# Optimization experiments

Hardware: AMD Instinct MI355X
Metric: run time of the kernel (lower is better)

The kernel has to match this reference:

```python
import jax, jax.numpy as jnp
import numpy as np

B, N, D = 32, 2048, 512

def setup_inputs() -> dict:
    key = jax.random.key(0)
    k1, k2, k3, k4 = jax.random.split(key, 4)
    return {
        "src": jax.random.normal(k1, (B, N, 3), dtype=jnp.float32),
        "tgt": jax.random.normal(k2, (B, N, 3), dtype=jnp.float32),
        "src_embed": jax.random.normal(k3, (B, N, D), dtype=jnp.float32),
        "tgt_embed": jax.random.normal(k4, (B, N, D), dtype=jnp.float32),
    }

def reference(src, tgt, src_embed, tgt_embed):
    # src, tgt: (B, N, 3); src_embed, tgt_embed: (B, N, D)
    d_k = jnp.asarray(src_embed.shape[-1], dtype=src_embed.dtype)
    # attention scores (B, N_src, N_tgt), softmax over tgt points
    scores = jnp.einsum('bnd,bmd->bnm', src_embed, tgt_embed) / jnp.sqrt(d_k)
    pointer = jax.nn.softmax(scores, axis=2)
    # matched = tgt^T @ pointer^T -> (B, 3, N_src)
    matched = jnp.einsum('bmc,bnm->bcn', tgt, pointer)
    src_t = jnp.transpose(src, (0, 2, 1))  # (B, 3, N)
    src_cent = jnp.mean(src_t, axis=2, keepdims=True)        # (B, 3, 1)
    matched_cent = jnp.mean(matched, axis=2, keepdims=True)  # (B, 3, 1)
    src_demean = src_t - src_cent
    matched_demean = matched - matched_cent
    # cross-covariance H: (B, 3, 3)
    H = jnp.einsum('bcn,bdn->bcd', src_demean, matched_demean)
    U, _, Vh = jnp.linalg.svd(H, full_matrices=False)  # square 3x3: reduced == full
    V = jnp.transpose(Vh, (0, 2, 1))
    R = jnp.matmul(V, jnp.transpose(U, (0, 2, 1)))
    det = jnp.linalg.det(R)
    identity = jnp.eye(3, dtype=R.dtype)
    reflect = jnp.diag(jnp.array([1.0, 1.0, -1.0], dtype=R.dtype))
    refl = jnp.where((det >= 0)[:, None, None], identity, reflect)
    R = jnp.matmul(refl, R)
    t = jnp.matmul(-R, src_cent) + matched_cent  # (B, 3, 1)
    t = jnp.transpose(t, (0, 2, 1))              # (B, 1, 3)
    return (R, t)
```

## Files before the change

kernel.cpp:

```cpp
#include <hip/hip_runtime.h>
#include <hip/hip_fp16.h>
#include <math.h>

#define B_ 32
#define N_ 2048
#define D_ 512
#define NT 256

typedef __attribute__((ext_vector_type(8))) _Float16 f16x8;
typedef __attribute__((ext_vector_type(8))) short s16x8;
typedef __attribute__((ext_vector_type(4))) float f32x4;
typedef __attribute__((ext_vector_type(4))) unsigned int u32x4;

__device__ inline unsigned packh2(float lo, float hi) {
    __half l = __float2half_rn(lo), h = __float2half_rn(hi);
    return (unsigned)__half_as_ushort(l) | ((unsigned)__half_as_ushort(h) << 16);
}
__device__ inline unsigned f2bf(float x) {
    unsigned u = __float_as_uint(x);
    return (u + 0x7FFFu + ((u >> 16) & 1u)) >> 16;
}
__device__ inline float bf2f(unsigned h) { return __uint_as_float(h << 16); }

__global__ __launch_bounds__(256) void prepass_kernel(
    const float* __restrict__ te, u32x4* __restrict__ kp)
{
    const int idx = blockIdx.x * 256 + threadIdx.x;
    const int b   = idx >> 17;
    const int r17 = idx & 131071;
    const int mt  = r17 >> 13;
    const int kt  = (r17 >> 9) & 15;
    const int o16 = r17 & 511;
    const int r   = o16 >> 2;
    const int s   = o16 & 3;
    const int lg  = s ^ ((r >> 1) & 3);
    const float* src = te + (((size_t)b * N_ + mt * 128 + r) * D_ + kt * 32 + lg * 8);
    const float4 f0 = *(const float4*)src;
    const float4 f1 = *(const float4*)(src + 4);
    u32x4 u;
    u[0] = packh2(f0.x, f0.y);
    u[1] = packh2(f0.z, f0.w);
    u[2] = packh2(f1.x, f1.y);
    u[3] = packh2(f1.z, f1.w);
    kp[idx] = u;
}

__global__ __launch_bounds__(NT, 2) void attn_db_kernel(
    const float* __restrict__ src, const float* __restrict__ tgt,
    const float* __restrict__ src_embed, const u32x4* __restrict__ kp,
    float* __restrict__ partials)
{
    __shared__ f16x8 Kbuf[2][4][512];
    __shared__ float4 TsB[2][128];
    __shared__ double red[4][15];

    const int tid  = threadIdx.x;
    const int wv   = tid >> 6;
    const int lane = tid & 63;
    const int lr   = lane & 15;
    const int lg   = lane >> 4;
    const int sxb  = (lg ^ ((lr >> 1) & 3)) << 4;
    char* KbufB = (char*)&Kbuf[0][0][0];

    const int xcd  = blockIdx.x & 7;
    const int idx  = blockIdx.x >> 3;
    const int b    = xcd * 4 + (idx >> 4);
    const int msl  = idx & 15;
    const int n0   = msl * 128;
    const int pblk = b * 16 + msl;

    const float QSC = 0.044194173824159216f * 1.4426950408889634f;
    f16x8 Qr[2][16];
#pragma unroll
    for (int qf = 0; qf < 2; ++qf) {
        const int qrow = n0 + wv * 32 + qf * 16 + lr;
        const float* qp = src_embed + ((size_t)b * N_ + qrow) * D_ + lg * 8;
#pragma unroll
        for (int s = 0; s < 16; ++s) {
            const float4 f0 = *(const float4*)(qp + s * 32);
            const float4 f1 = *(const float4*)(qp + s * 32 + 4);
            u32x4 u;
            u[0] = packh2(f0.x * QSC, f0.y * QSC);
            u[1] = packh2(f0.z * QSC, f0.w * QSC);
            u[2] = packh2(f1.x * QSC, f1.y * QSC);
            u[3] = packh2(f1.z * QSC, f1.w * QSC);
            Qr[qf][s] = __builtin_bit_cast(f16x8, u);
        }
    }
    if (tid < 128) {
        const float* tp = tgt + ((size_t)b * N_ + tid) * 3;
        TsB[0][tid] = make_float4(tp[0], tp[1], tp[2], 0.f);
    }

#define STAGE_TILE(t_, half_, ti_) do {                                        \
    const u32x4* _g = kp +                                                     \
        ((((size_t)b * 16 + ((t_) >> 4)) * 16 + ((t_) & 15)) << 9);            \
    __builtin_amdgcn_global_load_lds(                                          \
        (const __attribute__((address_space(1))) void*)(_g + tid),             \
        (__attribute__((address_space(3))) void*)(&Kbuf[half_][ti_][wv * 64]), \
        16, 0, 0);                                                             \
    __builtin_amdgcn_global_load_lds(                                          \
        (const __attribute__((address_space(1))) void*)(_g + 256 + tid),       \
        (__attribute__((address_space(3))) void*)(&Kbuf[half_][ti_][256 + wv * 64]),\
        16, 0, 0);                                                             \
} while (0)

#define STAGE_GROUP(gi_, half_) do {                                           \
    STAGE_TILE(4 * (gi_) + 0, half_, 0);                                       \
    STAGE_TILE(4 * (gi_) + 1, half_, 1);                                       \
    STAGE_TILE(4 * (gi_) + 2, half_, 2);                                       \
    STAGE_TILE(4 * (gi_) + 3, half_, 3);                                       \
} while (0)

    STAGE_GROUP(0, 0);

    float m_s[2] = {-1e30f, -1e30f}, l_s[2] = {0.f, 0.f};
    float axs[2] = {0.f, 0.f}, ays[2] = {0.f, 0.f}, azs[2] = {0.f, 0.f};

    f32x4 acc0[8], acc1[8];

    for (int g4 = 0; g4 < 16; ++g4) {
#pragma unroll
        for (int gm = 0; gm < 4; ++gm) {
            const int g = (g4 << 2) | gm;
            __syncthreads();
            if (g < 63) {
                const int gn = g + 1;
                STAGE_GROUP(gn, gn & 1);
            }
            float tv0 = 0.f, tv1 = 0.f, tv2 = 0.f;
            const bool pf = (gm == 3) && (g4 < 15) && (tid < 128);
            if (pf) {
                const float* tp = tgt + ((size_t)b * N_ + (g4 + 1) * 128 + tid) * 3;
                tv0 = tp[0]; tv1 = tp[1]; tv2 = tp[2];
            }
            if (gm == 0) {
#pragma unroll
                for (int nf = 0; nf < 8; ++nf) {
                    acc0[nf] = (f32x4){0.f, 0.f, 0.f, 0.f};
                    acc1[nf] = (f32x4){0.f, 0.f, 0.f, 0.f};
                }
            }
            __builtin_amdgcn_s_setprio(1);
#pragma unroll
            for (int ti = 0; ti < 4; ++ti) {
                const int kt = (gm << 2) | ti;
                const char* abase = KbufB + ((g & 1) << 15) + (ti << 13)
                                  + lr * 64 + sxb;
#pragma unroll
                for (int nf = 0; nf < 8; ++nf) {
                    const f16x8 a = *(const f16x8*)(abase + nf * 1024);
                    acc0[nf] = __builtin_amdgcn_mfma_f32_16x16x32_f16(a, Qr[0][kt], acc0[nf], 0, 0, 0);
                    acc1[nf] = __builtin_amdgcn_mfma_f32_16x16x32_f16(a, Qr[1][kt], acc1[nf], 0, 0, 0);
                }
            }
            __builtin_amdgcn_s_setprio(0);
            if (pf)
                TsB[(g4 + 1) & 1][tid] = make_float4(tv0, tv1, tv2, 0.f);

            if (gm == 3) {
                const float4* Ts = &TsB[g4 & 1][0];
                float mx0 = -1e30f, mx1 = -1e30f;
#pragma unroll
                for (int nf = 0; nf < 8; ++nf)
#pragma unroll
                    for (int r4 = 0; r4 < 4; ++r4) {
                        mx0 = fmaxf(mx0, acc0[nf][r4]);
                        mx1 = fmaxf(mx1, acc1[nf][r4]);
                    }
                mx0 = fmaxf(mx0, __shfl_xor(mx0, 16)); mx0 = fmaxf(mx0, __shfl_xor(mx0, 32));
                mx1 = fmaxf(mx1, __shfl_xor(mx1, 16)); mx1 = fmaxf(mx1, __shfl_xor(mx1, 32));
                const float mn0 = fmaxf(m_s[0], mx0), mn1 = fmaxf(m_s[1], mx1);
                const float c0 = exp2f(m_s[0] - mn0), c1 = exp2f(m_s[1] - mn1);
                l_s[0] *= c0; axs[0] *= c0; ays[0] *= c0; azs[0] *= c0; m_s[0] = mn0;
                l_s[1] *= c1; axs[1] *= c1; ays[1] *= c1; azs[1] *= c1; m_s[1] = mn1;
                float l0 = 0.f, x0 = 0.f, y0 = 0.f, z0 = 0.f;
                float l1 = 0.f, x1 = 0.f, y1 = 0.f, z1 = 0.f;
#pragma unroll
                for (int nf = 0; nf < 8; ++nf)
#pragma unroll
                    for (int r4 = 0; r4 < 4; ++r4) {
                        const float4 tv = Ts[nf * 16 + lg * 4 + r4];
                        const float p0 = exp2f(acc0[nf][r4] - mn0);
                        const float p1 = exp2f(acc1[nf][r4] - mn1);
                        l0 += p0; x0 = fmaf(p0, tv.x, x0); y0 = fmaf(p0, tv.y, y0); z0 = fmaf(p0, tv.z, z0);
                        l1 += p1; x1 = fmaf(p1, tv.x, x1); y1 = fmaf(p1, tv.y, y1); z1 = fmaf(p1, tv.z, z1);
                    }
                l_s[0] += l0; axs[0] += x0; ays[0] += y0; azs[0] += z0;
                l_s[1] += l1; axs[1] += x1; ays[1] += y1; azs[1] += z1;
            }
        }
    }
#undef STAGE_GROUP
#undef STAGE_TILE

    double dl[15];
#pragma unroll
    for (int i = 0; i < 15; ++i) dl[i] = 0.0;
#pragma unroll
    for (int qf = 0; qf < 2; ++qf) {
        float lt = l_s[qf], x = axs[qf], y = ays[qf], z = azs[qf];
        lt += __shfl_xor(lt, 16); lt += __shfl_xor(lt, 32);
        x  += __shfl_xor(x, 16);  x  += __shfl_xor(x, 32);
        y  += __shfl_xor(y, 16);  y  += __shfl_xor(y, 32);
        z  += __shfl_xor(z, 16);  z  += __shfl_xor(z, 32);
        if (lg == 0) {
            const int qrow = n0 + wv * 32 + qf * 16 + lr;
            const float* sp = src + ((size_t)b * N_ + qrow) * 3;
            const double inv = 1.0 / (double)lt;
            const double m0d = (double)x * inv, m1d = (double)y * inv, m2d = (double)z * inv;
            const double s0 = sp[0], s1 = sp[1], s2 = sp[2];
            dl[0] += s0;  dl[1] += s1;  dl[2] += s2;
            dl[3] += m0d; dl[4] += m1d; dl[5] += m2d;
            dl[6]  += s0 * m0d; dl[7]  += s0 * m1d; dl[8]  += s0 * m2d;
            dl[9]  += s1 * m0d; dl[10] += s1 * m1d; dl[11] += s1 * m2d;
            dl[12] += s2 * m0d; dl[13] += s2 * m1d; dl[14] += s2 * m2d;
        }
    }
#pragma unroll
    for (int i = 0; i < 15; ++i) {
        double v = dl[i];
        for (int off = 1; off < 64; off <<= 1) v += __shfl_xor(v, off);
        dl[i] = v;
    }
    if (lane == 0) {
#pragma unroll
        for (int i = 0; i < 15; ++i) red[wv][i] = dl[i];
    }
    __syncthreads();
    if (tid < 15) {
        double sum = 0.0;
        for (int w = 0; w < 4; ++w) sum += red[w][tid];
        partials[(size_t)pblk * 15 + tid] = (float)sum;
    }
}

__global__ __launch_bounds__(256, 2) void attn_v2_kernel(
    const float* __restrict__ src, const float* __restrict__ tgt,
    const float* __restrict__ src_embed, const float* __restrict__ tgt_embed,
    float* __restrict__ partials)
{
    __shared__ short Khi_s[128 * 64];
    __shared__ short Klo_s[128 * 64];
    __shared__ float4 Ts4[128];
    __shared__ double red[64][15];

    char* KhiB = (char*)Khi_s;
    char* KloB = (char*)Klo_s;

    const int w    = blockIdx.x;
    const int xcd  = w & 7;
    const int idx  = w >> 3;
    const int b    = xcd * 4 + (idx >> 5);
    const int n0   = (idx & 31) * 64;
    const int blk  = b * 32 + (idx & 31);

    const int tid  = threadIdx.x;
    const int wv   = tid >> 6;
    const int lane = tid & 63;
    const int lr   = lane & 15;
    const int lg   = lane >> 4;
    const unsigned swl = (unsigned)((lr & 7) << 4);

    const float scale = 0.044194173824159216f;
    const float* kbase = tgt_embed + (size_t)b * N_ * D_;

    const int qrow = n0 + wv * 16 + lr;
    const float* qp = src_embed + ((size_t)b * N_ + qrow) * D_ + lg * 8;
    s16x8 qhi[16], qlo[16];
#pragma unroll
    for (int s = 0; s < 16; ++s) {
        const float4 f0 = *reinterpret_cast<const float4*>(qp + s * 32);
        const float4 f1 = *reinterpret_cast<const float4*>(qp + s * 32 + 4);
        const float x[8] = {f0.x, f0.y, f0.z, f0.w, f1.x, f1.y, f1.z, f1.w};
#pragma unroll
        for (int i = 0; i < 8; ++i) {
            const float v = x[i] * scale;
            const unsigned h = f2bf(v);
            qhi[s][i] = (short)h;
            qlo[s][i] = (short)f2bf(v - bf2f(h));
        }
    }

    float m_run = -1e30f, l_run = 0.f, a0 = 0.f, a1 = 0.f, a2 = 0.f;
    const int srow = tid >> 1;
    const int shalf = tid & 1;
    const unsigned swr = (unsigned)((srow & 7) << 4);

    for (int m0 = 0; m0 < N_; m0 += 128) {
        f32x4 acc[8];
#pragma unroll
        for (int nf = 0; nf < 8; ++nf) acc[nf] = (f32x4){0.f, 0.f, 0.f, 0.f};

#pragma unroll
        for (int kt = 0; kt < 8; ++kt) {
            __syncthreads();
            {
                const float* gp = kbase + (size_t)(m0 + srow) * D_ + kt * 64 + shalf * 32;
#pragma unroll
                for (int grp = 0; grp < 4; ++grp) {
                    const float4 fa = *reinterpret_cast<const float4*>(gp + grp * 8);
                    const float4 fb = *reinterpret_cast<const float4*>(gp + grp * 8 + 4);
                    const float x[8] = {fa.x, fa.y, fa.z, fa.w, fb.x, fb.y, fb.z, fb.w};
                    s16x8 hi, lo;
#pragma unroll
                    for (int i = 0; i < 8; ++i) {
                        const unsigned h = f2bf(x[i]);
                        hi[i] = (short)h;
                        lo[i] = (short)f2bf(x[i] - bf2f(h));
                    }
                    const unsigned off = (unsigned)srow * 128u +
                        (((unsigned)(shalf * 64 + grp * 16)) ^ swr);
                    *reinterpret_cast<s16x8*>(KhiB + off) = hi;
                    *reinterpret_cast<s16x8*>(KloB + off) = lo;
                }
                if (kt == 0 && tid < 128) {
                    const float* tp = tgt + ((size_t)b * N_ + m0 + tid) * 3;
                    Ts4[tid] = make_float4(tp[0], tp[1], tp[2], 0.f);
                }
            }
            __syncthreads();
#pragma unroll
            for (int ks = 0; ks < 2; ++ks) {
                const int s = kt * 2 + ks;
                const unsigned kb = ((unsigned)(lg * 16 + ks * 64)) ^ swl;
#pragma unroll
                for (int nf = 0; nf < 8; ++nf) {
                    const unsigned off = (unsigned)(nf * 16 + lr) * 128u + kb;
                    const s16x8 ah = *reinterpret_cast<const s16x8*>(KhiB + off);
                    const s16x8 al = *reinterpret_cast<const s16x8*>(KloB + off);
                    acc[nf] = __builtin_amdgcn_mfma_f32_16x16x32_bf16(ah, qhi[s], acc[nf], 0, 0, 0);
                    acc[nf] = __builtin_amdgcn_mfma_f32_16x16x32_bf16(al, qhi[s], acc[nf], 0, 0, 0);
                    acc[nf] = __builtin_amdgcn_mfma_f32_16x16x32_bf16(ah, qlo[s], acc[nf], 0, 0, 0);
                }
            }
        }

        float mx = -1e30f;
#pragma unroll
        for (int nf = 0; nf < 8; ++nf)
#pragma unroll
            for (int r = 0; r < 4; ++r) mx = fmaxf(mx, acc[nf][r]);
        mx = fmaxf(mx, __shfl_xor(mx, 16));
        mx = fmaxf(mx, __shfl_xor(mx, 32));

        const float mnew = fmaxf(m_run, mx);
        const float corr = __expf(m_run - mnew);
        l_run *= corr; a0 *= corr; a1 *= corr; a2 *= corr;

        float ps = 0.f, p0 = 0.f, p1 = 0.f, p2 = 0.f;
#pragma unroll
        for (int nf = 0; nf < 8; ++nf)
#pragma unroll
            for (int r = 0; r < 4; ++r) {
                const float p = __expf(acc[nf][r] - mnew);
                const int n = nf * 16 + lg * 4 + r;
                const float4 tv = Ts4[n];
                ps += p;
                p0 = fmaf(p, tv.x, p0);
                p1 = fmaf(p, tv.y, p1);
                p2 = fmaf(p, tv.z, p2);
            }
        l_run += ps; a0 += p0; a1 += p1; a2 += p2;
        m_run = mnew;
    }

    l_run += __shfl_xor(l_run, 16); l_run += __shfl_xor(l_run, 32);
    a0 += __shfl_xor(a0, 16); a0 += __shfl_xor(a0, 32);
    a1 += __shfl_xor(a1, 16); a1 += __shfl_xor(a1, 32);
    a2 += __shfl_xor(a2, 16); a2 += __shfl_xor(a2, 32);

    __syncthreads();
    if (lg == 0) {
        const float inv = 1.0f / l_run;
        const double mx0 = (double)(a0 * inv);
        const double mx1 = (double)(a1 * inv);
        const double mx2 = (double)(a2 * inv);
        const float* sp = src + ((size_t)b * N_ + qrow) * 3;
        const double s0 = sp[0], s1 = sp[1], s2 = sp[2];
        double* rp = red[wv * 16 + lr];
        rp[0] = s0;  rp[1] = s1;  rp[2] = s2;
        rp[3] = mx0; rp[4] = mx1; rp[5] = mx2;
        rp[6]  = s0 * mx0; rp[7]  = s0 * mx1; rp[8]  = s0 * mx2;
        rp[9]  = s1 * mx0; rp[10] = s1 * mx1; rp[11] = s1 * mx2;
        rp[12] = s2 * mx0; rp[13] = s2 * mx1; rp[14] = s2 * mx2;
    }
    __syncthreads();
    if (tid < 15) {
        double sum = 0.0;
        for (int j = 0; j < 64; ++j) sum += red[j][tid];
        partials[(size_t)blk * 15 + tid] = (float)sum;
    }
}

__global__ void kabsch_kernel(const float* __restrict__ partials,
                              float* __restrict__ out, int nbb)
{
    const int b = threadIdx.x;
    if (b >= B_) return;

    double acc[15];
#pragma unroll
    for (int i = 0; i < 15; ++i) acc[i] = 0.0;
    for (int rb = 0; rb < nbb; ++rb) {
        const float* p = partials + ((size_t)b * nbb + rb) * 15;
#pragma unroll
        for (int i = 0; i < 15; ++i) acc[i] += (double)p[i];
    }

    const double invN = 1.0 / (double)N_;
    const double S[3] = {acc[0], acc[1], acc[2]};
    const double M[3] = {acc[3], acc[4], acc[5]};
    double H[3][3];
    for (int c = 0; c < 3; ++c)
        for (int d = 0; d < 3; ++d)
            H[c][d] = acc[6 + c * 3 + d] - S[c] * M[d] * invN;

    double A[3][3];
    for (int i = 0; i < 3; ++i)
        for (int j = 0; j < 3; ++j)
            A[i][j] = H[0][i] * H[0][j] + H[1][i] * H[1][j] + H[2][i] * H[2][j];

    double V[3][3] = {{1, 0, 0}, {0, 1, 0}, {0, 0, 1}};
    const int PQ[3][2] = {{0, 1}, {0, 2}, {1, 2}};
    for (int sweep = 0; sweep < 20; ++sweep) {
        const double off = fabs(A[0][1]) + fabs(A[0][2]) + fabs(A[1][2]);
        if (off < 1e-24) break;
        for (int pi = 0; pi < 3; ++pi) {
            const int p = PQ[pi][0], q = PQ[pi][1], rr = 3 - p - q;
            const double apq = A[p][q];
            if (fabs(apq) < 1e-300) continue;
            const double theta = (A[q][q] - A[p][p]) / (2.0 * apq);
            const double tt = (theta >= 0.0 ? 1.0 : -1.0) /
                              (fabs(theta) + sqrt(1.0 + theta * theta));
            const double c = 1.0 / sqrt(1.0 + tt * tt);
            const double sn = tt * c;
            const double app = A[p][p], aqq = A[q][q];
            const double arp = A[rr][p], arq = A[rr][q];
            A[p][p] = app - tt * apq;
            A[q][q] = aqq + tt * apq;
            A[p][q] = A[q][p] = 0.0;
            A[rr][p] = A[p][rr] = c * arp - sn * arq;
            A[rr][q] = A[q][rr] = sn * arp + c * arq;
            for (int k = 0; k < 3; ++k) {
                const double vkp = V[k][p], vkq = V[k][q];
                V[k][p] = c * vkp - sn * vkq;
                V[k][q] = sn * vkp + c * vkq;
            }
        }
    }

    double R[3][3] = {{0, 0, 0}, {0, 0, 0}, {0, 0, 0}};
    for (int i = 0; i < 3; ++i) {
        const double lam = A[i][i];
        const double sig = sqrt(lam > 0.0 ? lam : 0.0);
        const double inv = 1.0 / (sig > 1e-30 ? sig : 1e-30);
        double wv[3];
        for (int c = 0; c < 3; ++c)
            wv[c] = H[c][0] * V[0][i] + H[c][1] * V[1][i] + H[c][2] * V[2][i];
        for (int r = 0; r < 3; ++r)
            for (int c = 0; c < 3; ++c)
                R[r][c] += V[r][i] * wv[c] * inv;
    }

    const double det =
        R[0][0] * (R[1][1] * R[2][2] - R[1][2] * R[2][1]) -
        R[0][1] * (R[1][0] * R[2][2] - R[1][2] * R[2][0]) +
        R[0][2] * (R[1][0] * R[2][1] - R[1][1] * R[2][0]);
    if (det < 0.0) {
        R[2][0] = -R[2][0]; R[2][1] = -R[2][1]; R[2][2] = -R[2][2];
    }

    double t[3];
    for (int c = 0; c < 3; ++c)
        t[c] = M[c] * invN -
               (R[c][0] * S[0] + R[c][1] * S[1] + R[c][2] * S[2]) * invN;

    for (int r = 0; r < 3; ++r)
        for (int c = 0; c < 3; ++c)
            out[(size_t)b * 9 + r * 3 + c] = (float)R[r][c];
    for (int c = 0; c < 3; ++c)
        out[(size_t)B_ * 9 + (size_t)b * 3 + c] = (float)t[c];
}

extern "C" void kernel_launch(void* const* d_in, const int* in_sizes, int n_in,
                              void* d_out, int out_size, void* d_ws, size_t ws_size,
                              hipStream_t stream) {
    const float* src = (const float*)d_in[0];
    const float* tgt = (const float*)d_in[1];
    const float* se  = (const float*)d_in[2];
    const float* te  = (const float*)d_in[3];
    float* out = (float*)d_out;

    const size_t KP_OFF = 32768;
    const size_t need = KP_OFF + (size_t)B_ * N_ * D_ * 2;

    if (ws_size >= need) {
        u32x4* kp = (u32x4*)((char*)d_ws + KP_OFF);
        prepass_kernel<<<dim3(16384), dim3(256), 0, stream>>>(te, kp);
        attn_db_kernel<<<dim3(512), dim3(NT), 0, stream>>>(
            src, tgt, se, kp, (float*)d_ws);
        kabsch_kernel<<<dim3(1), dim3(64), 0, stream>>>((float*)d_ws, out, 16);
    } else {
        attn_v2_kernel<<<dim3(1024), dim3(256), 0, stream>>>(
            src, tgt, se, te, (float*)d_ws);
        kabsch_kernel<<<dim3(1), dim3(64), 0, stream>>>((float*)d_ws, out, 32);
    }
}
```

Baseline: 226.5 us.

## Switch attention scores to 32x32x16 MFMA tiles per wave

Replaces the paired 16x16x32 MFMA fragments with a single 32x32x16 MFMA layout, so each wave computes a 32-query by 128-key tile with four 16-wide accumulator vectors. Q fragments, the K swizzled LDS addressing, the softmax row/column mapping and the final reductions are remapped for the new lane layout. The aim is fewer LDS reads per MFMA and fewer instructions per FLOP; in exchange it changes register pressure and the LDS access pattern.

```diff
diff --git a/kernel.cpp b/kernel.cpp
--- a/kernel.cpp
+++ b/kernel.cpp
@@ -10,6 +10,7 @@
 typedef __attribute__((ext_vector_type(8))) _Float16 f16x8;
 typedef __attribute__((ext_vector_type(8))) short s16x8;
 typedef __attribute__((ext_vector_type(4))) float f32x4;
+typedef __attribute__((ext_vector_type(16))) float f32x16;
 typedef __attribute__((ext_vector_type(4))) unsigned int u32x4;
 
 __device__ inline unsigned packh2(float lo, float hi) {
@@ -45,7 +46,7 @@
     kp[idx] = u;
 }
 
-__global__ __launch_bounds__(NT, 2) void attn_db_kernel(
+__global__ __launch_bounds__(NT, 2) void attn_db32_kernel(
     const float* __restrict__ src, const float* __restrict__ tgt,
     const float* __restrict__ src_embed, const u32x4* __restrict__ kp,
     float* __restrict__ partials)
@@ -57,10 +58,13 @@
     const int tid  = threadIdx.x;
     const int wv   = tid >> 6;
     const int lane = tid & 63;
-    const int lr   = lane & 15;
-    const int lg   = lane >> 4;
-    const int sxb  = (lg ^ ((lr >> 1) & 3)) << 4;
+    const int lr   = lane & 31;
+    const int hi   = lane >> 5;
     char* KbufB = (char*)&Kbuf[0][0][0];
+
+    const int sw   = (lr >> 1) & 3;
+    const int sxb0 = ((0 + hi) ^ sw) << 4;
+    const int sxb1 = ((2 + hi) ^ sw) << 4;
 
     const int xcd  = blockIdx.x & 7;
     const int idx  = blockIdx.x >> 3;
@@ -70,21 +74,20 @@
     const int pblk = b * 16 + msl;
 
     const float QSC = 0.044194173824159216f * 1.4426950408889634f;
-    f16x8 Qr[2][16];
-#pragma unroll
-    for (int qf = 0; qf < 2; ++qf) {
-        const int qrow = n0 + wv * 32 + qf * 16 + lr;
-        const float* qp = src_embed + ((size_t)b * N_ + qrow) * D_ + lg * 8;
-#pragma unroll
-        for (int s = 0; s < 16; ++s) {
-            const float4 f0 = *(const float4*)(qp + s * 32);
-            const float4 f1 = *(const float4*)(qp + s * 32 + 4);
+    const int qrow = n0 + wv * 32 + lr;
+    f16x8 Qr[32];
+    {
+        const float* qp = src_embed + ((size_t)b * N_ + qrow) * D_ + hi * 8;
+#pragma unroll
+        for (int s = 0; s < 32; ++s) {
+            const float4 f0 = *(const float4*)(qp + s * 16);
+            const float4 f1 = *(const float4*)(qp + s * 16 + 4);
             u32x4 u;
             u[0] = packh2(f0.x * QSC, f0.y * QSC);
             u[1] = packh2(f0.z * QSC, f0.w * QSC);
             u[2] = packh2(f1.x * QSC, f1.y * QSC);
             u[3] = packh2(f1.z * QSC, f1.w * QSC);
-            Qr[qf][s] = __builtin_bit_cast(f16x8, u);
+            Qr[s] = __builtin_bit_cast(f16x8, u);
         }
     }
     if (tid < 128) {
@@ -114,10 +117,8 @@
 
     STAGE_GROUP(0, 0);
 
-    float m_s[2] = {-1e30f, -1e30f}, l_s[2] = {0.f, 0.f};
-    float axs[2] = {0.f, 0.f}, ays[2] = {0.f, 0.f}, azs[2] = {0.f, 0.f};
-
-    f32x4 acc0[8], acc1[8];
+    float m_s = -1e30f, l_s = 0.f, axs = 0.f, ays = 0.f, azs = 0.f;
+    f32x16 acc[4];
 
     for (int g4 = 0; g4 < 16; ++g4) {
 #pragma unroll
@@ -136,22 +137,25 @@
             }
             if (gm == 0) {
 #pragma unroll
-                for (int nf = 0; nf < 8; ++nf) {
-                    acc0[nf] = (f32x4){0.f, 0.f, 0.f, 0.f};
-                    acc1[nf] = (f32x4){0.f, 0.f, 0.f, 0.f};
-                }
-            }
+                for (int rg = 0; rg < 4; ++rg)
+#pragma unroll
+                    for (int r16 = 0; r16 < 16; ++r16) acc[rg][r16] = 0.f;
+            }
+            const char* gbase = KbufB + ((g & 1) << 15) + lr * 64;
             __builtin_amdgcn_s_setprio(1);
 #pragma unroll
             for (int ti = 0; ti < 4; ++ti) {
-                const int kt = (gm << 2) | ti;
-                const char* abase = KbufB + ((g & 1) << 15) + (ti << 13)
-                                  + lr * 64 + sxb;
-#pragma unroll
-                for (int nf = 0; nf < 8; ++nf) {
-                    const f16x8 a = *(const f16x8*)(abase + nf * 1024);
-                    acc0[nf] = __builtin_amdgcn_mfma_f32_16x16x32_f16(a, Qr[0][kt], acc0[nf], 0, 0, 0);
-                    acc1[nf] = __builtin_amdgcn_mfma_f32_16x16x32_f16(a, Qr[1][kt], acc1[nf], 0, 0, 0);
+                const char* tb = gbase + (ti << 13);
+#pragma unroll
+                for (int kh = 0; kh < 2; ++kh) {
+                    const int sxb = kh ? sxb1 : sxb0;
+                    const f16x8 q = Qr[(((gm << 2) | ti) << 1) | kh];
+#pragma unroll
+                    for (int rg = 0; rg < 4; ++rg) {
+                        const f16x8 a = *(const f16x8*)(tb + rg * 2048 + sxb);
+                        acc[rg] = __builtin_amdgcn_mfma_f32_32x32x16_f16(
+                            a, q, acc[rg], 0, 0, 0);
+                    }
                 }
             }
             __builtin_amdgcn_s_setprio(0);
@@ -160,62 +164,56 @@
 
             if (gm == 3) {
                 const float4* Ts = &TsB[g4 & 1][0];
-                float mx0 = -1e30f, mx1 = -1e30f;
-#pragma unroll
-                for (int nf = 0; nf < 8; ++nf)
-#pragma unroll
-                    for (int r4 = 0; r4 < 4; ++r4) {
-                        mx0 = fmaxf(mx0, acc0[nf][r4]);
-                        mx1 = fmaxf(mx1, acc1[nf][r4]);
+                float mx = -1e30f;
+#pragma unroll
+                for (int rg = 0; rg < 4; ++rg)
+#pragma unroll
+                    for (int r16 = 0; r16 < 16; ++r16)
+                        mx = fmaxf(mx, acc[rg][r16]);
+                mx = fmaxf(mx, __shfl_xor(mx, 32));
+                const float mn = fmaxf(m_s, mx);
+                const float c  = exp2f(m_s - mn);
+                l_s *= c; axs *= c; ays *= c; azs *= c; m_s = mn;
+                float l0 = 0.f, x0 = 0.f, y0 = 0.f, z0 = 0.f;
+#pragma unroll
+                for (int rg = 0; rg < 4; ++rg)
+#pragma unroll
+                    for (int r16 = 0; r16 < 16; ++r16) {
+                        const int kr = (r16 & 3) + 8 * (r16 >> 2) + 4 * hi + 32 * rg;
+                        const float4 tv = Ts[kr];
+                        const float p = exp2f(acc[rg][r16] - mn);
+                        l0 += p;
+                        x0 = fmaf(p, tv.x, x0);
+                        y0 = fmaf(p, tv.y, y0);
+                        z0 = fmaf(p, tv.z, z0);
                     }
-                mx0 = fmaxf(mx0, __shfl_xor(mx0, 16)); mx0 = fmaxf(mx0, __shfl_xor(mx0, 32));
-                mx1 = fmaxf(mx1, __shfl_xor(mx1, 16)); mx1 = fmaxf(mx1, __shfl_xor(mx1, 32));
-                const float mn0 = fmaxf(m_s[0], mx0), mn1 = fmaxf(m_s[1], mx1);
-                const float c0 = exp2f(m_s[0] - mn0), c1 = exp2f(m_s[1] - mn1);
-                l_s[0] *= c0; axs[0] *= c0; ays[0] *= c0; azs[0] *= c0; m_s[0] = mn0;
-                l_s[1] *= c1; axs[1] *= c1; ays[1] *= c1; azs[1] *= c1; m_s[1] = mn1;
-                float l0 = 0.f, x0 = 0.f, y0 = 0.f, z0 = 0.f;
-                float l1 = 0.f, x1 = 0.f, y1 = 0.f, z1 = 0.f;
-#pragma unroll
-                for (int nf = 0; nf < 8; ++nf)
-#pragma unroll
-                    for (int r4 = 0; r4 < 4; ++r4) {
-                        const float4 tv = Ts[nf * 16 + lg * 4 + r4];
-                        const float p0 = exp2f(acc0[nf][r4] - mn0);
-                        const float p1 = exp2f(acc1[nf][r4] - mn1);
-                        l0 += p0; x0 = fmaf(p0, tv.x, x0); y0 = fmaf(p0, tv.y, y0); z0 = fmaf(p0, tv.z, z0);
-                        l1 += p1; x1 = fmaf(p1, tv.x, x1); y1 = fmaf(p1, tv.y, y1); z1 = fmaf(p1, tv.z, z1);
-                    }
-                l_s[0] += l0; axs[0] += x0; ays[0] += y0; azs[0] += z0;
-                l_s[1] += l1; axs[1] += x1; ays[1] += y1; azs[1] += z1;
+                l_s += l0; axs += x0; ays += y0; azs += z0;
             }
         }
     }
 #undef STAGE_GROUP
 #undef STAGE_TILE
 
+    l_s += __shfl_xor(l_s, 32);
+    axs += __shfl_xor(axs, 32);
+    ays += __shfl_xor(ays, 32);
+    azs += __shfl_xor(azs, 32);
+
     double dl[15];
 #pragma unroll
     for (int i = 0; i < 15; ++i) dl[i] = 0.0;
-#pragma unroll
-    for (int qf = 0; qf < 2; ++qf) {
-        float lt = l_s[qf], x = axs[qf], y = ays[qf], z = azs[qf];
-        lt += __shfl_xor(lt, 16); lt += __shfl_xor(lt, 32);
-        x  += __shfl_xor(x, 16);  x  += __shfl_xor(x, 32);
-        y  += __shfl_xor(y, 16);  y  += __shfl_xor(y, 32);
-        z  += __shfl_xor(z, 16);  z  += __shfl_xor(z, 32);
-        if (lg == 0) {
-            const int qrow = n0 + wv * 32 + qf * 16 + lr;
-            const float* sp = src + ((size_t)b * N_ + qrow) * 3;
-            const double inv = 1.0 / (double)lt;
-            const double m0d = (double)x * inv, m1d = (double)y * inv, m2d = (double)z * inv;
-            const double s0 = sp[0], s1 = sp[1], s2 = sp[2];
-            dl[0] += s0;  dl[1] += s1;  dl[2] += s2;
-            dl[3] += m0d; dl[4] += m1d; dl[5] += m2d;
-            dl[6]  += s0 * m0d; dl[7]  += s0 * m1d; dl[8]  += s0 * m2d;
-            dl[9]  += s1 * m0d; dl[10] += s1 * m1d; dl[11] += s1 * m2d;
-            dl[12] += s2 * m0d; dl[13] += s2 * m1d; dl[14] += s2 * m2d;
-        }
+    if (hi == 0) {
+        const float* sp = src + ((size_t)b * N_ + qrow) * 3;
+        const double inv = 1.0 / (double)l_s;
+        const double m0d = (double)axs * inv;
+        const double m1d = (double)ays * inv;
+        const double m2d = (double)azs * inv;
+        const double s0 = sp[0], s1 = sp[1], s2 = sp[2];
+        dl[0] = s0;  dl[1] = s1;  dl[2] = s2;
+        dl[3] = m0d; dl[4] = m1d; dl[5] = m2d;
+        dl[6]  = s0 * m0d; dl[7]  = s0 * m1d; dl[8]  = s0 * m2d;
+        dl[9]  = s1 * m0d; dl[10] = s1 * m1d; dl[11] = s1 * m2d;
+        dl[12] = s2 * m0d; dl[13] = s2 * m1d; dl[14] = s2 * m2d;
     }
 #pragma unroll
     for (int i = 0; i < 15; ++i) {
@@ -498,7 +496,7 @@
     if (ws_size >= need) {
         u32x4* kp = (u32x4*)((char*)d_ws + KP_OFF);
         prepass_kernel<<<dim3(16384), dim3(256), 0, stream>>>(te, kp);
-        attn_db_kernel<<<dim3(512), dim3(NT), 0, stream>>>(
+        attn_db32_kernel<<<dim3(512), dim3(NT), 0, stream>>>(
             src, tgt, se, kp, (float*)d_ws);
         kabsch_kernel<<<dim3(1), dim3(64), 0, stream>>>((float*)d_ws, out, 16);
     } else {
```

New measurement: 233.6 us. 3.1% more time.

## Split attention over key halves with merge kernel and streamed Q fragments

Applied to the files above, without the earlier changes.

The attention kernel now splits each query block's key range into two halves, doubling the grid to 1024 blocks. Each block writes per-row running max, sum and weighted coordinates, and a new merge kernel combines the two halves before the covariance reduction. Q fragments are no longer held in registers for all of D; they are loaded and converted per k-tile in a software pipeline, which lowers register pressure (launch bounds raised to 3 blocks per CU) and halves the LDS K buffer. The cost is an extra kernel launch, a small intermediate buffer, and Q being reloaded from global memory for every key tile pass.

```diff
diff --git a/kernel.cpp b/kernel.cpp
--- a/kernel.cpp
+++ b/kernel.cpp
@@ -5,7 +5,6 @@
 #define B_ 32
 #define N_ 2048
 #define D_ 512
-#define NT 256
 
 typedef __attribute__((ext_vector_type(8))) _Float16 f16x8;
 typedef __attribute__((ext_vector_type(8))) short s16x8;
@@ -45,14 +44,12 @@
     kp[idx] = u;
 }
 
-__global__ __launch_bounds__(NT, 2) void attn_db_kernel(
-    const float* __restrict__ src, const float* __restrict__ tgt,
-    const float* __restrict__ src_embed, const u32x4* __restrict__ kp,
-    float* __restrict__ partials)
+__global__ __launch_bounds__(256, 3) void attn_kv_kernel(
+    const float* __restrict__ tgt, const float* __restrict__ src_embed,
+    const u32x4* __restrict__ kp, float* __restrict__ mlv)
 {
-    __shared__ f16x8 Kbuf[2][4][512];
+    __shared__ f16x8 Kbuf[2][2][512];
     __shared__ float4 TsB[2][128];
-    __shared__ double red[4][15];
 
     const int tid  = threadIdx.x;
     const int wv   = tid >> 6;
@@ -64,77 +61,88 @@
 
     const int xcd  = blockIdx.x & 7;
     const int idx  = blockIdx.x >> 3;
-    const int b    = xcd * 4 + (idx >> 4);
-    const int msl  = idx & 15;
+    const int b    = xcd * 4 + (idx >> 5);
+    const int r5   = idx & 31;
+    const int msl  = r5 >> 1;
+    const int kvh  = r5 & 1;
     const int n0   = msl * 128;
-    const int pblk = b * 16 + msl;
+    const int mc0  = kvh * 8;
 
     const float QSC = 0.044194173824159216f * 1.4426950408889634f;
-    f16x8 Qr[2][16];
-#pragma unroll
-    for (int qf = 0; qf < 2; ++qf) {
-        const int qrow = n0 + wv * 32 + qf * 16 + lr;
-        const float* qp = src_embed + ((size_t)b * N_ + qrow) * D_ + lg * 8;
-#pragma unroll
-        for (int s = 0; s < 16; ++s) {
-            const float4 f0 = *(const float4*)(qp + s * 32);
-            const float4 f1 = *(const float4*)(qp + s * 32 + 4);
-            u32x4 u;
-            u[0] = packh2(f0.x * QSC, f0.y * QSC);
-            u[1] = packh2(f0.z * QSC, f0.w * QSC);
-            u[2] = packh2(f1.x * QSC, f1.y * QSC);
-            u[3] = packh2(f1.z * QSC, f1.w * QSC);
-            Qr[qf][s] = __builtin_bit_cast(f16x8, u);
-        }
-    }
-    if (tid < 128) {
-        const float* tp = tgt + ((size_t)b * N_ + tid) * 3;
-        TsB[0][tid] = make_float4(tp[0], tp[1], tp[2], 0.f);
-    }
-
-#define STAGE_TILE(t_, half_, ti_) do {                                        \
-    const u32x4* _g = kp +                                                     \
-        ((((size_t)b * 16 + ((t_) >> 4)) * 16 + ((t_) & 15)) << 9);            \
+    const float* qp0 = src_embed + ((size_t)b * N_ + n0 + wv * 32 + lr) * D_ + lg * 8;
+    const float* qp1 = qp0 + (size_t)16 * D_;
+
+    f16x8 Qc0, Qc1;
+    float4 qb0, qb1, qb2, qb3;
+
+#define QLOAD(t_) do {                                                         \
+    const int _ko = ((t_) & 15) * 32;                                          \
+    qb0 = *(const float4*)(qp0 + _ko);                                         \
+    qb1 = *(const float4*)(qp0 + _ko + 4);                                     \
+    qb2 = *(const float4*)(qp1 + _ko);                                         \
+    qb3 = *(const float4*)(qp1 + _ko + 4);                                     \
+} while (0)
+
+#define QCVT() do {                                                            \
+    u32x4 _u;                                                                  \
+    _u[0] = packh2(qb0.x * QSC, qb0.y * QSC);                                  \
+    _u[1] = packh2(qb0.z * QSC, qb0.w * QSC);                                  \
+    _u[2] = packh2(qb1.x * QSC, qb1.y * QSC);                                  \
+    _u[3] = packh2(qb1.z * QSC, qb1.w * QSC);                                  \
+    Qc0 = __builtin_bit_cast(f16x8, _u);                                       \
+    _u[0] = packh2(qb2.x * QSC, qb2.y * QSC);                                  \
+    _u[1] = packh2(qb2.z * QSC, qb2.w * QSC);                                  \
+    _u[2] = packh2(qb3.x * QSC, qb3.y * QSC);                                  \
+    _u[3] = packh2(qb3.z * QSC, qb3.w * QSC);                                  \
+    Qc1 = __builtin_bit_cast(f16x8, _u);                                       \
+} while (0)
+
+#define STAGE_TILE(t_) do {                                                    \
+    const int _mc = mc0 + ((t_) >> 4);                                         \
+    const u32x4* _g = kp + ((((size_t)b * 16 + _mc) * 16 + ((t_) & 15)) << 9); \
+    f16x8* _d = &Kbuf[((t_) >> 1) & 1][(t_) & 1][wv * 64];                     \
     __builtin_amdgcn_global_load_lds(                                          \
         (const __attribute__((address_space(1))) void*)(_g + tid),             \
-        (__attribute__((address_space(3))) void*)(&Kbuf[half_][ti_][wv * 64]), \
-        16, 0, 0);                                                             \
+        (__attribute__((address_space(3))) void*)_d, 16, 0, 0);                \
     __builtin_amdgcn_global_load_lds(                                          \
         (const __attribute__((address_space(1))) void*)(_g + 256 + tid),       \
-        (__attribute__((address_space(3))) void*)(&Kbuf[half_][ti_][256 + wv * 64]),\
-        16, 0, 0);                                                             \
+        (__attribute__((address_space(3))) void*)(_d + 256), 16, 0, 0);        \
 } while (0)
 
-#define STAGE_GROUP(gi_, half_) do {                                           \
-    STAGE_TILE(4 * (gi_) + 0, half_, 0);                                       \
-    STAGE_TILE(4 * (gi_) + 1, half_, 1);                                       \
-    STAGE_TILE(4 * (gi_) + 2, half_, 2);                                       \
-    STAGE_TILE(4 * (gi_) + 3, half_, 3);                                       \
-} while (0)
-
-    STAGE_GROUP(0, 0);
+    QLOAD(0); QCVT(); QLOAD(1);
+    STAGE_TILE(0); STAGE_TILE(1);
+    if (tid < 128) {
+        const float* tp = tgt + ((size_t)b * N_ + mc0 * 128 + tid) * 3;
+        TsB[0][tid] = make_float4(tp[0], tp[1], tp[2], 0.f);
+    }
 
     float m_s[2] = {-1e30f, -1e30f}, l_s[2] = {0.f, 0.f};
     float axs[2] = {0.f, 0.f}, ays[2] = {0.f, 0.f}, azs[2] = {0.f, 0.f};
-
     f32x4 acc0[8], acc1[8];
 
-    for (int g4 = 0; g4 < 16; ++g4) {
-#pragma unroll
-        for (int gm = 0; gm < 4; ++gm) {
-            const int g = (g4 << 2) | gm;
+#define MFMA_TILE(halfb_, ti_) do {                                            \
+    const char* _ab = KbufB + (halfb_) * 16384 + (ti_) * 8192 + lr * 64 + sxb; \
+    _Pragma("unroll")                                                          \
+    for (int nf = 0; nf < 8; ++nf) {                                           \
+        const f16x8 a = *(const f16x8*)(_ab + nf * 1024);                      \
+        acc0[nf] = __builtin_amdgcn_mfma_f32_16x16x32_f16(a, Qc0, acc0[nf], 0, 0, 0); \
+        acc1[nf] = __builtin_amdgcn_mfma_f32_16x16x32_f16(a, Qc1, acc1[nf], 0, 0, 0); \
+    }                                                                          \
+} while (0)
+
+    for (int mcl = 0; mcl < 8; ++mcl) {
+        for (int g = 0; g < 8; ++g) {
+            const int t = (mcl << 4) | (g << 1);
             __syncthreads();
-            if (g < 63) {
-                const int gn = g + 1;
-                STAGE_GROUP(gn, gn & 1);
-            }
+            if (t < 126) { STAGE_TILE(t + 2); STAGE_TILE(t + 3); }
             float tv0 = 0.f, tv1 = 0.f, tv2 = 0.f;
-            const bool pf = (gm == 3) && (g4 < 15) && (tid < 128);
+            const bool pf = (g == 7) && (mcl < 7) && (tid < 128);
             if (pf) {
-                const float* tp = tgt + ((size_t)b * N_ + (g4 + 1) * 128 + tid) * 3;
+                const float* tp = tgt +
+                    ((size_t)b * N_ + (mc0 + mcl + 1) * 128 + tid) * 3;
                 tv0 = tp[0]; tv1 = tp[1]; tv2 = tp[2];
             }
-            if (gm == 0) {
+            if (g == 0) {
 #pragma unroll
                 for (int nf = 0; nf < 8; ++nf) {
                     acc0[nf] = (f32x4){0.f, 0.f, 0.f, 0.f};
@@ -142,24 +150,18 @@
                 }
             }
             __builtin_amdgcn_s_setprio(1);
-#pragma unroll
-            for (int ti = 0; ti < 4; ++ti) {
-                const int kt = (gm << 2) | ti;
-                const char* abase = KbufB + ((g & 1) << 15) + (ti << 13)
-                                  + lr * 64 + sxb;
-#pragma unroll
-                for (int nf = 0; nf < 8; ++nf) {
-                    const f16x8 a = *(const f16x8*)(abase + nf * 1024);
-                    acc0[nf] = __builtin_amdgcn_mfma_f32_16x16x32_f16(a, Qr[0][kt], acc0[nf], 0, 0, 0);
-                    acc1[nf] = __builtin_amdgcn_mfma_f32_16x16x32_f16(a, Qr[1][kt], acc1[nf], 0, 0, 0);
-                }
-            }
+            MFMA_TILE(g & 1, 0);
+            QCVT();
+            QLOAD(t + 2);
+            MFMA_TILE(g & 1, 1);
+            QCVT();
+            QLOAD(t + 3);
             __builtin_amdgcn_s_setprio(0);
             if (pf)
-                TsB[(g4 + 1) & 1][tid] = make_float4(tv0, tv1, tv2, 0.f);
-
-            if (gm == 3) {
-                const float4* Ts = &TsB[g4 & 1][0];
+                TsB[(mcl + 1) & 1][tid] = make_float4(tv0, tv1, tv2, 0.f);
+
+            if (g == 7) {
+                const float4* Ts = &TsB[mcl & 1][0];
                 float mx0 = -1e30f, mx1 = -1e30f;
 #pragma unroll
                 for (int nf = 0; nf < 8; ++nf)
@@ -191,12 +193,11 @@
             }
         }
     }
-#undef STAGE_GROUP
+#undef MFMA_TILE
 #undef STAGE_TILE
-
-    double dl[15];
-#pragma unroll
-    for (int i = 0; i < 15; ++i) dl[i] = 0.0;
+#undef QCVT
+#undef QLOAD
+
 #pragma unroll
     for (int qf = 0; qf < 2; ++qf) {
         float lt = l_s[qf], x = axs[qf], y = ays[qf], z = azs[qf];
@@ -205,18 +206,50 @@
         y  += __shfl_xor(y, 16);  y  += __shfl_xor(y, 32);
         z  += __shfl_xor(z, 16);  z  += __shfl_xor(z, 32);
         if (lg == 0) {
-            const int qrow = n0 + wv * 32 + qf * 16 + lr;
-            const float* sp = src + ((size_t)b * N_ + qrow) * 3;
-            const double inv = 1.0 / (double)lt;
-            const double m0d = (double)x * inv, m1d = (double)y * inv, m2d = (double)z * inv;
-            const double s0 = sp[0], s1 = sp[1], s2 = sp[2];
-            dl[0] += s0;  dl[1] += s1;  dl[2] += s2;
-            dl[3] += m0d; dl[4] += m1d; dl[5] += m2d;
-            dl[6]  += s0 * m0d; dl[7]  += s0 * m1d; dl[8]  += s0 * m2d;
-            dl[9]  += s1 * m0d; dl[10] += s1 * m1d; dl[11] += s1 * m2d;
-            dl[12] += s2 * m0d; dl[13] += s2 * m1d; dl[14] += s2 * m2d;
+            const int row = wv * 32 + qf * 16 + lr;
+            float* rp = mlv +
+                (((size_t)(b * 16 + msl) * 2 + kvh) * 128 + row) * 5;
+            rp[0] = m_s[qf]; rp[1] = lt; rp[2] = x; rp[3] = y; rp[4] = z;
         }
     }
+}
+
+__global__ void merge_kernel(const float* __restrict__ src,
+                             const float* __restrict__ mlv,
+                             float* __restrict__ partials)
+{
+    __shared__ double red[2][15];
+    const int blk = blockIdx.x;
+    const int b   = blk >> 4;
+    const int msl = blk & 15;
+    const int tid = threadIdx.x;
+    const int wv  = tid >> 6;
+    const int lane = tid & 63;
+
+    const float* r0 = mlv + ((size_t)blk * 2 + 0) * 128 * 5 + (size_t)tid * 5;
+    const float* r1 = mlv + ((size_t)blk * 2 + 1) * 128 * 5 + (size_t)tid * 5;
+    const float m0 = r0[0], l0f = r0[1], x0 = r0[2], y0 = r0[3], z0 = r0[4];
+    const float m1 = r1[0], l1f = r1[1], x1 = r1[2], y1 = r1[3], z1 = r1[4];
+    const float M  = fmaxf(m0, m1);
+    const double w0 = (double)exp2f(m0 - M), w1 = (double)exp2f(m1 - M);
+    const double l  = (double)l0f * w0 + (double)l1f * w1;
+    const double ax = (double)x0 * w0 + (double)x1 * w1;
+    const double ay = (double)y0 * w0 + (double)y1 * w1;
+    const double az = (double)z0 * w0 + (double)z1 * w1;
+    const double inv = 1.0 / l;
+    const double m0d = ax * inv, m1d = ay * inv, m2d = az * inv;
+
+    const int n = msl * 128 + tid;
+    const float* sp = src + ((size_t)b * N_ + n) * 3;
+    const double s0 = sp[0], s1 = sp[1], s2 = sp[2];
+
+    double dl[15];
+    dl[0] = s0;  dl[1] = s1;  dl[2] = s2;
+    dl[3] = m0d; dl[4] = m1d; dl[5] = m2d;
+    dl[6]  = s0 * m0d; dl[7]  = s0 * m1d; dl[8]  = s0 * m2d;
+    dl[9]  = s1 * m0d; dl[10] = s1 * m1d; dl[11] = s1 * m2d;
+    dl[12] = s2 * m0d; dl[13] = s2 * m1d; dl[14] = s2 * m2d;
+
 #pragma unroll
     for (int i = 0; i < 15; ++i) {
         double v = dl[i];
@@ -228,11 +261,8 @@
         for (int i = 0; i < 15; ++i) red[wv][i] = dl[i];
     }
     __syncthreads();
-    if (tid < 15) {
-        double sum = 0.0;
-        for (int w = 0; w < 4; ++w) sum += red[w][tid];
-        partials[(size_t)pblk * 15 + tid] = (float)sum;
-    }
+    if (tid < 15)
+        partials[(size_t)blk * 15 + tid] = (float)(red[0][tid] + red[1][tid]);
 }
 
 __global__ __launch_bounds__(256, 2) void attn_v2_kernel(
@@ -492,14 +522,17 @@
     const float* te  = (const float*)d_in[3];
     float* out = (float*)d_out;
 
-    const size_t KP_OFF = 32768;
-    const size_t need = KP_OFF + (size_t)B_ * N_ * D_ * 2;
+    const size_t MLV_OFF = 32768;
+    const size_t MLV_SZ  = (size_t)1024 * 128 * 5 * 4;
+    const size_t KP_OFF  = MLV_OFF + MLV_SZ;
+    const size_t need    = KP_OFF + (size_t)B_ * N_ * D_ * 2;
 
     if (ws_size >= need) {
-        u32x4* kp = (u32x4*)((char*)d_ws + KP_OFF);
+        u32x4* kp  = (u32x4*)((char*)d_ws + KP_OFF);
+        float* mlv = (float*)((char*)d_ws + MLV_OFF);
         prepass_kernel<<<dim3(16384), dim3(256), 0, stream>>>(te, kp);
-        attn_db_kernel<<<dim3(512), dim3(NT), 0, stream>>>(
-            src, tgt, se, kp, (float*)d_ws);
+        attn_kv_kernel<<<dim3(1024), dim3(256), 0, stream>>>(tgt, se, kp, mlv);
+        merge_kernel<<<dim3(512), dim3(128), 0, stream>>>(src, mlv, (float*)d_ws);
         kabsch_kernel<<<dim3(1), dim3(64), 0, stream>>>((float*)d_ws, out, 16);
     } else {
         attn_v2_kernel<<<dim3(1024), dim3(256), 0, stream>>>(
```

New measurement: 462.0 us. +104.0%, slower.
